# Kernel optimization log

Hardware: AMD Instinct MI355X
Metric: run time of the kernel (lower is better)

The kernel has to match this reference:

```python
import jax, jax.numpy as jnp
import numpy as np

N = 100000   # nodes
E = 1600000  # edges
D = 128      # feature dim (all layer_sizes equal)


def setup_inputs() -> dict:
    key = jax.random.key(0)
    ks = jax.random.split(key, 8)
    s = 1.0 / np.sqrt(D)
    return {
        "x": jax.random.normal(ks[0], (N, D), jnp.float32),
        "edge_index": jax.random.randint(ks[1], (2, E), 0, N, dtype=jnp.int32),
        "W1": jax.random.normal(ks[2], (D, D), jnp.float32) * s,  # GCNConv.lin weight [out,in]
        "b1": jnp.zeros((D,), jnp.float32),
        "a1": jnp.full((1,), 0.25, jnp.float32),  # PReLU slope (torch default)
        "W2": jax.random.normal(ks[3], (D, D), jnp.float32) * s,
        "b2": jnp.zeros((D,), jnp.float32),
        "a2": jnp.full((1,), 0.25, jnp.float32),
    }


def _gcn_conv(x, W, b, row, col, norm):
    # linear transform then normalized scatter-add aggregation
    h = x @ W.T + b                      # [N, D]
    msg = h[row] * norm[:, None]         # [E+N, D] gather + scale
    return jax.ops.segment_sum(msg, col, num_segments=N) # [N, D]


def _prelu(y, a):
    return jnp.where(y > 0, y, a * y)


def reference(x, edge_index, W1, b1, a1, W2, b2, a2):
    src, dst = edge_index[0], edge_index[1]
    loop = jnp.arange(N, dtype=src.dtype)
    # add self loops (GCNConv default add_self_loops=True)
    row = jnp.concatenate([src, loop])
    col = jnp.concatenate([dst, loop])
    # symmetric normalization: deg^{-1/2}[row] * deg^{-1/2}[col]
    deg = jax.ops.segment_sum(jnp.ones_like(col, dtype=x.dtype), col, num_segments=N)
    dis = jnp.where(deg > 0, jax.lax.rsqrt(deg), 0.0)
    norm = dis[row] * dis[col]
    # layer 1: GCNConv -> Identity (batchnorm=False) -> PReLU
    h = _prelu(_gcn_conv(x, W1, b1, row, col, norm), a1)
    # layer 2
    h = _prelu(_gcn_conv(h, W2, b2, row, col, norm), a2)
    return h
```

## Files before the change

### kernel.cpp

```cpp
#include <hip/hip_runtime.h>
#include <hip/hip_fp16.h>

#define D 128
#define PCH 4096

typedef _Float16 half_t;
typedef _Float16 f16x8 __attribute__((ext_vector_type(8)));
typedef _Float16 f16x4 __attribute__((ext_vector_type(4)));
typedef float    f32x4 __attribute__((ext_vector_type(4)));

__global__ __launch_bounds__(256) void k_histw(const int* __restrict__ dstv, int* bcnt,
                                               int e, int nb,
                                               const float* __restrict__ W1,
                                               const float* __restrict__ W2,
                                               half_t* __restrict__ Wh) {
    if (blockIdx.x >= 512) {
        int q = (blockIdx.x - 512) * 256 + threadIdx.x;
        if (q < 8192) {
            const float4* src = (q < 4096) ? (const float4*)W1 : (const float4*)W2;
            float4 v = src[q & 4095];
            f16x4 h;
            h[0] = (_Float16)v.x; h[1] = (_Float16)v.y;
            h[2] = (_Float16)v.z; h[3] = (_Float16)v.w;
            ((f16x4*)Wh)[q] = h;
        }
        return;
    }
    __shared__ int h[512];
    for (int i = threadIdx.x; i < nb; i += 256) h[i] = 0;
    __syncthreads();
    const int stride = 512 * 256;
    for (int i = blockIdx.x * 256 + threadIdx.x; i < e; i += stride)
        atomicAdd(&h[dstv[i] >> 8], 1);
    __syncthreads();
    for (int i = threadIdx.x; i < nb; i += 256)
        if (h[i]) atomicAdd(&bcnt[i], h[i]);
}

__global__ __launch_bounds__(512) void k_bscan(const int* __restrict__ bcnt, int* bbase,
                                               int* bcur, int nb, int e) {
    __shared__ int sd[512];
    int t = threadIdx.x;
    int v = (t < nb) ? bcnt[t] : 0;
    sd[t] = v;
    __syncthreads();
    for (int off = 1; off < 512; off <<= 1) {
        int x = (t >= off) ? sd[t - off] : 0;
        __syncthreads();
        sd[t] += x;
        __syncthreads();
    }
    int excl = sd[t] - v;
    if (t < nb) { bbase[t] = excl; bcur[t] = excl; }
    if (t == nb - 1) bbase[nb] = e;
}

__global__ __launch_bounds__(512) void k_part(const int* __restrict__ srcv,
                                              const int* __restrict__ dstv,
                                              int* bcur, unsigned int* __restrict__ ebuf,
                                              int e, int nb) {
    __shared__ int h[512];
    __shared__ int base[512];
    int c0 = blockIdx.x * PCH;
    int c1 = min(c0 + PCH, e);
    for (int i = threadIdx.x; i < nb; i += 512) h[i] = 0;
    __syncthreads();
    for (int i = c0 + threadIdx.x; i < c1; i += 512)
        atomicAdd(&h[dstv[i] >> 8], 1);
    __syncthreads();
    for (int i = threadIdx.x; i < nb; i += 512) {
        int c = h[i];
        base[i] = c ? atomicAdd(&bcur[i], c) : 0;
    }
    __syncthreads();
    for (int i = threadIdx.x; i < nb; i += 512) h[i] = 0;
    __syncthreads();
    for (int i = c0 + threadIdx.x; i < c1; i += 512) {
        int d = dstv[i];
        int b = d >> 8;
        int pos = atomicAdd(&h[b], 1);
        ebuf[base[b] + pos] = ((unsigned int)srcv[i] << 8) | (unsigned int)(d & 255);
    }
}

__global__ __launch_bounds__(512) void k_bucket(const unsigned int* __restrict__ ebuf,
                                                const int* __restrict__ bbase,
                                                int* __restrict__ rowptr,
                                                int* __restrict__ csr_src,
                                                float* __restrict__ dis, int n, int e) {
    __shared__ int cnt[256];
    __shared__ int off[256];
    int b = blockIdx.x;
    int t = threadIdx.x;
    int s0 = bbase[b], s1 = bbase[b + 1];
    if (t < 256) cnt[t] = 0;
    __syncthreads();
    for (int i = s0 + t; i < s1; i += 512)
        atomicAdd(&cnt[ebuf[i] & 255], 1);
    __syncthreads();
    int v = (t < 256) ? cnt[t] : 0;
    if (t < 256) off[t] = v;
    __syncthreads();
    for (int o = 1; o < 256; o <<= 1) {
        int x = (t >= o && t < 256) ? off[t - o] : 0;
        __syncthreads();
        if (t < 256) off[t] += x;
        __syncthreads();
    }
    if (t < 256) {
        int excl = off[t] - v;
        int node = b * 256 + t;
        if (node < n) {
            rowptr[node] = s0 + excl;
            dis[node] = rsqrtf((float)(v + 1));
        }
        if (b == 0 && t == 0) rowptr[n] = e;
        cnt[t] = excl;
    }
    __syncthreads();
    for (int i = s0 + t; i < s1; i += 512) {
        unsigned int u = ebuf[i];
        int pos = atomicAdd(&cnt[u & 255], 1);
        csr_src[s0 + pos] = (int)(u >> 8);
    }
}

template<bool FP16IN>
__global__ __launch_bounds__(512) void k_gemm(const void* __restrict__ Xv,
                                              const half_t* __restrict__ Wh,
                                              const float* __restrict__ B,
                                              const float* __restrict__ dis,
                                              half_t* __restrict__ Gh, int n) {
    __shared__ _Float16 lds[128 * 136];
    const int t = threadIdx.x;
    const int row0 = blockIdx.x * 128;

    #pragma unroll
    for (int i = 0; i < 4; ++i) {
        int gid = i * 512 + t;
        int row = gid >> 4, g = gid & 15;
        int grow = row0 + row;
        int so = ((g ^ (row & 7)) * 8);
        f16x8 hv;
        if constexpr (FP16IN) {
            uint4 u = make_uint4(0, 0, 0, 0);
            if (grow < n) u = ((const uint4*)Xv)[(size_t)grow * 16 + g];
            hv = *(f16x8*)&u;
        } else {
            float4 a = make_float4(0.f, 0.f, 0.f, 0.f);
            float4 b = make_float4(0.f, 0.f, 0.f, 0.f);
            if (grow < n) {
                a = ((const float4*)Xv)[(size_t)grow * 32 + g * 2];
                b = ((const float4*)Xv)[(size_t)grow * 32 + g * 2 + 1];
            }
            hv[0] = (_Float16)a.x; hv[1] = (_Float16)a.y;
            hv[2] = (_Float16)a.z; hv[3] = (_Float16)a.w;
            hv[4] = (_Float16)b.x; hv[5] = (_Float16)b.y;
            hv[6] = (_Float16)b.z; hv[7] = (_Float16)b.w;
        }
        *(f16x8*)&lds[row * 128 + so] = hv;
    }
    __syncthreads();

    const int w = t >> 6, l = t & 63;
    const int rbase = (w >> 1) * 32;
    const int cbase = (w & 1) * 64;
    const int lr = l & 15, lk = l >> 4;

    f32x4 acc[2][4] = {};

    #pragma unroll
    for (int kb = 0; kb < 4; ++kb) {
        f16x8 bf[4], af[2];
        #pragma unroll
        for (int ct = 0; ct < 4; ++ct) {
            int j = cbase + ct * 16 + lr;
            bf[ct] = *(const f16x8*)(Wh + j * 128 + kb * 32 + lk * 8);
        }
        #pragma unroll
        for (int rt = 0; rt < 2; ++rt) {
            int row = rbase + rt * 16 + lr;
            int G = kb * 4 + lk;
            af[rt] = *(const f16x8*)&lds[row * 128 + ((G ^ (row & 7)) * 8)];
        }
        #pragma unroll
        for (int rt = 0; rt < 2; ++rt)
            #pragma unroll
            for (int ct = 0; ct < 4; ++ct)
                acc[rt][ct] = __builtin_amdgcn_mfma_f32_16x16x32_f16(af[rt], bf[ct],
                                                                    acc[rt][ct], 0, 0, 0);
    }

    float bc[4];
    #pragma unroll
    for (int ct = 0; ct < 4; ++ct) bc[ct] = B[cbase + ct * 16 + lr];

    __syncthreads();
    #pragma unroll
    for (int rt = 0; rt < 2; ++rt)
        #pragma unroll
        for (int q = 0; q < 4; ++q) {
            int rl = rbase + rt * 16 + lk * 4 + q;
            int grow = row0 + rl;
            float ds = (grow < n) ? dis[grow] : 0.f;
            #pragma unroll
            for (int ct = 0; ct < 4; ++ct) {
                float v = (acc[rt][ct][q] + bc[ct]) * ds;
                lds[rl * 136 + cbase + ct * 16 + lr] = (_Float16)v;
            }
        }
    __syncthreads();
    #pragma unroll
    for (int i = 0; i < 4; ++i) {
        int gid = i * 512 + t;
        int row = gid >> 4, g = gid & 15;
        int grow = row0 + row;
        if (grow < n)
            *(f16x8*)&Gh[(size_t)grow * 128 + g * 8] = *(f16x8*)&lds[row * 136 + g * 8];
    }
}

template<bool FP16OUT>
__global__ __launch_bounds__(256) void k_gather(const half_t* __restrict__ G,
                                                const float* __restrict__ dis,
                                                const int* __restrict__ rowptr,
                                                const int* __restrict__ csr_src,
                                                const float* __restrict__ a,
                                                void* __restrict__ O, int n, int nquad) {
    int wq = (blockIdx.x * 256 + threadIdx.x) >> 6;
    if (wq >= nquad) return;
    int lane = threadIdx.x & 63;
    int node = wq * 4 + (lane >> 4);
    if (node >= n) node = n - 1;
    int sl = lane & 15;

    const uint4* Gv = (const uint4*)G;
    float ac[8];
    {
        uint4 su = Gv[(size_t)node * 16 + sl];
        f16x8 h = *(f16x8*)&su;
        #pragma unroll
        for (int j = 0; j < 8; ++j) ac[j] = (float)h[j];
    }

    int e = rowptr[node], e1 = rowptr[node + 1];
    for (; e + 4 <= e1; e += 4) {
        int s0 = csr_src[e + 0];
        int s1 = csr_src[e + 1];
        int s2 = csr_src[e + 2];
        int s3 = csr_src[e + 3];
        uint4 u0 = Gv[(size_t)s0 * 16 + sl];
        uint4 u1 = Gv[(size_t)s1 * 16 + sl];
        uint4 u2 = Gv[(size_t)s2 * 16 + sl];
        uint4 u3 = Gv[(size_t)s3 * 16 + sl];
        f16x8 h0 = *(f16x8*)&u0;
        f16x8 h1 = *(f16x8*)&u1;
        f16x8 h2 = *(f16x8*)&u2;
        f16x8 h3 = *(f16x8*)&u3;
        #pragma unroll
        for (int j = 0; j < 8; ++j)
            ac[j] += (float)h0[j] + (float)h1[j] + (float)h2[j] + (float)h3[j];
    }
    for (; e < e1; ++e) {
        int s = csr_src[e];
        uint4 u = Gv[(size_t)s * 16 + sl];
        f16x8 h = *(f16x8*)&u;
        #pragma unroll
        for (int j = 0; j < 8; ++j) ac[j] += (float)h[j];
    }

    float dsc = dis[node];
    float al = a[0];
    #pragma unroll
    for (int j = 0; j < 8; ++j) {
        float v = ac[j] * dsc;
        ac[j] = v > 0.f ? v : al * v;
    }
    if constexpr (FP16OUT) {
        f16x8 h;
        #pragma unroll
        for (int j = 0; j < 8; ++j) h[j] = (_Float16)ac[j];
        ((f16x8*)O)[(size_t)node * 16 + sl] = h;
    } else {
        float4 o0 = make_float4(ac[0], ac[1], ac[2], ac[3]);
        float4 o1 = make_float4(ac[4], ac[5], ac[6], ac[7]);
        ((float4*)O)[(size_t)node * 32 + sl * 2]     = o0;
        ((float4*)O)[(size_t)node * 32 + sl * 2 + 1] = o1;
    }
}

extern "C" void kernel_launch(void* const* d_in, const int* in_sizes, int n_in,
                              void* d_out, int out_size, void* d_ws, size_t ws_size,
                              hipStream_t stream) {
    const float* x  = (const float*)d_in[0];
    const int*   ei = (const int*)d_in[1];
    const float* W1 = (const float*)d_in[2];
    const float* b1 = (const float*)d_in[3];
    const float* a1 = (const float*)d_in[4];
    const float* W2 = (const float*)d_in[5];
    const float* b2 = (const float*)d_in[6];
    const float* a2 = (const float*)d_in[7];

    const int n = in_sizes[0] / D;
    const int e = in_sizes[1] / 2;
    const int* srcv = ei;
    const int* dstv = ei + e;
    const int nb = (n + 255) >> 8;

    char* ws = (char*)d_ws;
    size_t off = 0;
    auto alloc = [&](size_t bytes) {
        void* p = ws + off;
        off = (off + bytes + 255) & ~(size_t)255;
        return p;
    };
    float*        dis     = (float*)       alloc((size_t)n * 4);
    int*          rowptr  = (int*)         alloc((size_t)(n + 1) * 4);
    int*          csr_src = (int*)         alloc((size_t)e * 4);
    int*          bcnt    = (int*)         alloc(512 * 4);
    int*          bbase   = (int*)         alloc(513 * 4);
    int*          bcur    = (int*)         alloc(512 * 4);
    unsigned int* ebuf    = (unsigned int*)alloc((size_t)e * 4);
    half_t*       bufH    = (half_t*)      alloc((size_t)n * D * 2);
    half_t*       h1h     = (half_t*)      alloc((size_t)n * D * 2);
    half_t*       Wh      = (half_t*)      alloc(2 * 16384 * 2);

    dim3 blk(256);
    const int npart = (e + PCH - 1) / PCH;

    hipMemsetAsync(bcnt, 0, 512 * 4, stream);
    k_histw <<<544, blk, 0, stream>>>(dstv, bcnt, e, nb, W1, W2, Wh);
    k_bscan <<<1, 512, 0, stream>>>(bcnt, bbase, bcur, nb, e);
    k_part  <<<npart, 512, 0, stream>>>(srcv, dstv, bcur, ebuf, e, nb);
    k_bucket<<<nb, 512, 0, stream>>>(ebuf, bbase, rowptr, csr_src, dis, n, e);

    const int nquad = (n + 3) / 4;
    const int gat_grid = (nquad * 64 + 255) / 256;
    const int gemm_grid = (n + 127) / 128;

    k_gemm<false><<<gemm_grid, 512, 0, stream>>>(x, Wh, b1, dis, bufH, n);
    k_gather<true><<<gat_grid, blk, 0, stream>>>(bufH, dis, rowptr, csr_src, a1, h1h, n, nquad);
    k_gemm<true><<<gemm_grid, 512, 0, stream>>>(h1h, Wh + 16384, b2, dis, bufH, n);
    k_gather<false><<<gat_grid, blk, 0, stream>>>(bufH, dis, rowptr, csr_src, a2, d_out, n, nquad);
}
```

Baseline: 237.7 us.

## Fuse layer-1 gather with layer-2 GEMM and fold bucket scan into consumers

Folds the single-block bucket scan into k_part and k_bucket, which now each recompute the prefix sum of bucket counts redundantly. This removes one launch and the bbase buffer. It also fuses the layer-1 aggregation and PReLU with the layer-2 GEMM, so the aggregated features stay in LDS and are never written to and re-read from global memory. The cost is that the gather now runs at 128 rows per 512-thread block with a 16-lane-per-node layout, which may reduce the latency hiding available to the irregular gather loads.

Measured after the change: 245.6 us. 3.4% more time.

```diff
diff --git a/kernel.cpp b/kernel.cpp
--- a/kernel.cpp
+++ b/kernel.cpp
@@ -37,45 +37,42 @@
         if (h[i]) atomicAdd(&bcnt[i], h[i]);
 }
 
-__global__ __launch_bounds__(512) void k_bscan(const int* __restrict__ bcnt, int* bbase,
-                                               int* bcur, int nb, int e) {
+__global__ __launch_bounds__(512) void k_part(const int* __restrict__ srcv,
+                                              const int* __restrict__ dstv,
+                                              const int* __restrict__ bcnt,
+                                              int* bcur, unsigned int* __restrict__ ebuf,
+                                              int e, int nb) {
     __shared__ int sd[512];
+    __shared__ int bexcl[512];
+    __shared__ int h[512];
+    __shared__ int base[512];
     int t = threadIdx.x;
     int v = (t < nb) ? bcnt[t] : 0;
     sd[t] = v;
     __syncthreads();
-    for (int off = 1; off < 512; off <<= 1) {
-        int x = (t >= off) ? sd[t - off] : 0;
+    for (int o = 1; o < 512; o <<= 1) {
+        int x = (t >= o) ? sd[t - o] : 0;
         __syncthreads();
         sd[t] += x;
         __syncthreads();
     }
-    int excl = sd[t] - v;
-    if (t < nb) { bbase[t] = excl; bcur[t] = excl; }
-    if (t == nb - 1) bbase[nb] = e;
-}
-
-__global__ __launch_bounds__(512) void k_part(const int* __restrict__ srcv,
-                                              const int* __restrict__ dstv,
-                                              int* bcur, unsigned int* __restrict__ ebuf,
-                                              int e, int nb) {
-    __shared__ int h[512];
-    __shared__ int base[512];
+    bexcl[t] = sd[t] - v;
+    for (int i = t; i < nb; i += 512) h[i] = 0;
+    __syncthreads();
+
     int c0 = blockIdx.x * PCH;
     int c1 = min(c0 + PCH, e);
-    for (int i = threadIdx.x; i < nb; i += 512) h[i] = 0;
-    __syncthreads();
-    for (int i = c0 + threadIdx.x; i < c1; i += 512)
+    for (int i = c0 + t; i < c1; i += 512)
         atomicAdd(&h[dstv[i] >> 8], 1);
     __syncthreads();
-    for (int i = threadIdx.x; i < nb; i += 512) {
+    for (int i = t; i < nb; i += 512) {
         int c = h[i];
-        base[i] = c ? atomicAdd(&bcur[i], c) : 0;
-    }
-    __syncthreads();
-    for (int i = threadIdx.x; i < nb; i += 512) h[i] = 0;
-    __syncthreads();
-    for (int i = c0 + threadIdx.x; i < c1; i += 512) {
+        base[i] = c ? (bexcl[i] + atomicAdd(&bcur[i], c)) : 0;
+    }
+    __syncthreads();
+    for (int i = t; i < nb; i += 512) h[i] = 0;
+    __syncthreads();
+    for (int i = c0 + t; i < c1; i += 512) {
         int d = dstv[i];
         int b = d >> 8;
         int pos = atomicAdd(&h[b], 1);
@@ -84,15 +81,29 @@
 }
 
 __global__ __launch_bounds__(512) void k_bucket(const unsigned int* __restrict__ ebuf,
-                                                const int* __restrict__ bbase,
+                                                const int* __restrict__ bcnt,
                                                 int* __restrict__ rowptr,
                                                 int* __restrict__ csr_src,
-                                                float* __restrict__ dis, int n, int e) {
+                                                float* __restrict__ dis, int n, int e,
+                                                int nb) {
+    __shared__ int sd[512];
     __shared__ int cnt[256];
     __shared__ int off[256];
     int b = blockIdx.x;
     int t = threadIdx.x;
-    int s0 = bbase[b], s1 = bbase[b + 1];
+    int v0 = (t < nb) ? bcnt[t] : 0;
+    sd[t] = v0;
+    __syncthreads();
+    for (int o = 1; o < 512; o <<= 1) {
+        int x = (t >= o) ? sd[t - o] : 0;
+        __syncthreads();
+        sd[t] += x;
+        __syncthreads();
+    }
+    int s1 = sd[b];
+    int s0 = s1 - ((b < nb) ? bcnt[b] : 0);
+    __syncthreads();
+
     if (t < 256) cnt[t] = 0;
     __syncthreads();
     for (int i = s0 + t; i < s1; i += 512)
@@ -125,8 +136,7 @@
     }
 }
 
-template<bool FP16IN>
-__global__ __launch_bounds__(512) void k_gemm(const void* __restrict__ Xv,
+__global__ __launch_bounds__(512) void k_gemm(const float* __restrict__ Xv,
                                               const half_t* __restrict__ Wh,
                                               const float* __restrict__ B,
                                               const float* __restrict__ dis,
@@ -141,23 +151,17 @@
         int row = gid >> 4, g = gid & 15;
         int grow = row0 + row;
         int so = ((g ^ (row & 7)) * 8);
+        float4 a = make_float4(0.f, 0.f, 0.f, 0.f);
+        float4 b = make_float4(0.f, 0.f, 0.f, 0.f);
+        if (grow < n) {
+            a = ((const float4*)Xv)[(size_t)grow * 32 + g * 2];
+            b = ((const float4*)Xv)[(size_t)grow * 32 + g * 2 + 1];
+        }
         f16x8 hv;
-        if constexpr (FP16IN) {
-            uint4 u = make_uint4(0, 0, 0, 0);
-            if (grow < n) u = ((const uint4*)Xv)[(size_t)grow * 16 + g];
-            hv = *(f16x8*)&u;
-        } else {
-            float4 a = make_float4(0.f, 0.f, 0.f, 0.f);
-            float4 b = make_float4(0.f, 0.f, 0.f, 0.f);
-            if (grow < n) {
-                a = ((const float4*)Xv)[(size_t)grow * 32 + g * 2];
-                b = ((const float4*)Xv)[(size_t)grow * 32 + g * 2 + 1];
-            }
-            hv[0] = (_Float16)a.x; hv[1] = (_Float16)a.y;
-            hv[2] = (_Float16)a.z; hv[3] = (_Float16)a.w;
-            hv[4] = (_Float16)b.x; hv[5] = (_Float16)b.y;
-            hv[6] = (_Float16)b.z; hv[7] = (_Float16)b.w;
-        }
+        hv[0] = (_Float16)a.x; hv[1] = (_Float16)a.y;
+        hv[2] = (_Float16)a.z; hv[3] = (_Float16)a.w;
+        hv[4] = (_Float16)b.x; hv[5] = (_Float16)b.y;
+        hv[6] = (_Float16)b.z; hv[7] = (_Float16)b.w;
         *(f16x8*)&lds[row * 128 + so] = hv;
     }
     __syncthreads();
@@ -220,13 +224,137 @@
     }
 }
 
-template<bool FP16OUT>
+__global__ __launch_bounds__(512) void k_fusedg(const half_t* __restrict__ G1,
+                                                const float* __restrict__ dis,
+                                                const int* __restrict__ rowptr,
+                                                const int* __restrict__ csr_src,
+                                                const float* __restrict__ a,
+                                                const half_t* __restrict__ Wh,
+                                                const float* __restrict__ B,
+                                                half_t* __restrict__ G2, int n) {
+    __shared__ _Float16 lds[128 * 136];
+    const int t = threadIdx.x;
+    const int row0 = blockIdx.x * 128;
+    const int grp = t >> 4;
+    const int sl  = t & 15;
+    const float al = a[0];
+    const uint4* Gv = (const uint4*)G1;
+
+    #pragma unroll 1
+    for (int it = 0; it < 4; ++it) {
+        int rl = it * 32 + grp;
+        int node = row0 + rl;
+        float ac[8];
+        #pragma unroll
+        for (int j = 0; j < 8; ++j) ac[j] = 0.f;
+        if (node < n) {
+            uint4 su = Gv[(size_t)node * 16 + sl];
+            f16x8 h = *(f16x8*)&su;
+            #pragma unroll
+            for (int j = 0; j < 8; ++j) ac[j] = (float)h[j];
+            int e = rowptr[node], e1 = rowptr[node + 1];
+            for (; e + 4 <= e1; e += 4) {
+                int s0 = csr_src[e + 0];
+                int s1 = csr_src[e + 1];
+                int s2 = csr_src[e + 2];
+                int s3 = csr_src[e + 3];
+                uint4 u0 = Gv[(size_t)s0 * 16 + sl];
+                uint4 u1 = Gv[(size_t)s1 * 16 + sl];
+                uint4 u2 = Gv[(size_t)s2 * 16 + sl];
+                uint4 u3 = Gv[(size_t)s3 * 16 + sl];
+                f16x8 h0 = *(f16x8*)&u0;
+                f16x8 h1 = *(f16x8*)&u1;
+                f16x8 h2 = *(f16x8*)&u2;
+                f16x8 h3 = *(f16x8*)&u3;
+                #pragma unroll
+                for (int j = 0; j < 8; ++j)
+                    ac[j] += (float)h0[j] + (float)h1[j] + (float)h2[j] + (float)h3[j];
+            }
+            for (; e < e1; ++e) {
+                int s = csr_src[e];
+                uint4 u = Gv[(size_t)s * 16 + sl];
+                f16x8 h = *(f16x8*)&u;
+                #pragma unroll
+                for (int j = 0; j < 8; ++j) ac[j] += (float)h[j];
+            }
+            float dsc = dis[node];
+            #pragma unroll
+            for (int j = 0; j < 8; ++j) {
+                float v = ac[j] * dsc;
+                ac[j] = v > 0.f ? v : al * v;
+            }
+        }
+        f16x8 hv;
+        #pragma unroll
+        for (int j = 0; j < 8; ++j) hv[j] = (_Float16)ac[j];
+        *(f16x8*)&lds[rl * 128 + ((sl ^ (rl & 7)) * 8)] = hv;
+    }
+    __syncthreads();
+
+    const int w = t >> 6, l = t & 63;
+    const int rbase = (w >> 1) * 32;
+    const int cbase = (w & 1) * 64;
+    const int lr = l & 15, lk = l >> 4;
+
+    f32x4 acc[2][4] = {};
+
+    #pragma unroll
+    for (int kb = 0; kb < 4; ++kb) {
+        f16x8 bf[4], af[2];
+        #pragma unroll
+        for (int ct = 0; ct < 4; ++ct) {
+            int j = cbase + ct * 16 + lr;
+            bf[ct] = *(const f16x8*)(Wh + j * 128 + kb * 32 + lk * 8);
+        }
+        #pragma unroll
+        for (int rt = 0; rt < 2; ++rt) {
+            int row = rbase + rt * 16 + lr;
+            int G = kb * 4 + lk;
+            af[rt] = *(const f16x8*)&lds[row * 128 + ((G ^ (row & 7)) * 8)];
+        }
+        #pragma unroll
+        for (int rt = 0; rt < 2; ++rt)
+            #pragma unroll
+            for (int ct = 0; ct < 4; ++ct)
+                acc[rt][ct] = __builtin_amdgcn_mfma_f32_16x16x32_f16(af[rt], bf[ct],
+                                                                    acc[rt][ct], 0, 0, 0);
+    }
+
+    float bc[4];
+    #pragma unroll
+    for (int ct = 0; ct < 4; ++ct) bc[ct] = B[cbase + ct * 16 + lr];
+
+    __syncthreads();
+    #pragma unroll
+    for (int rt = 0; rt < 2; ++rt)
+        #pragma unroll
+        for (int q = 0; q < 4; ++q) {
+            int rl = rbase + rt * 16 + lk * 4 + q;
+            int grow = row0 + rl;
+            float ds = (grow < n) ? dis[grow] : 0.f;
+            #pragma unroll
+            for (int ct = 0; ct < 4; ++ct) {
+                float v = (acc[rt][ct][q] + bc[ct]) * ds;
+                lds[rl * 136 + cbase + ct * 16 + lr] = (_Float16)v;
+            }
+        }
+    __syncthreads();
+    #pragma unroll
+    for (int i = 0; i < 4; ++i) {
+        int gid = i * 512 + t;
+        int row = gid >> 4, g = gid & 15;
+        int grow = row0 + row;
+        if (grow < n)
+            *(f16x8*)&G2[(size_t)grow * 128 + g * 8] = *(f16x8*)&lds[row * 136 + g * 8];
+    }
+}
+
 __global__ __launch_bounds__(256) void k_gather(const half_t* __restrict__ G,
                                                 const float* __restrict__ dis,
                                                 const int* __restrict__ rowptr,
                                                 const int* __restrict__ csr_src,
                                                 const float* __restrict__ a,
-                                                void* __restrict__ O, int n, int nquad) {
+                                                float* __restrict__ O, int n, int nquad) {
     int wq = (blockIdx.x * 256 + threadIdx.x) >> 6;
     if (wq >= nquad) return;
     int lane = threadIdx.x & 63;
@@ -276,17 +404,10 @@
         float v = ac[j] * dsc;
         ac[j] = v > 0.f ? v : al * v;
     }
-    if constexpr (FP16OUT) {
-        f16x8 h;
-        #pragma unroll
-        for (int j = 0; j < 8; ++j) h[j] = (_Float16)ac[j];
-        ((f16x8*)O)[(size_t)node * 16 + sl] = h;
-    } else {
-        float4 o0 = make_float4(ac[0], ac[1], ac[2], ac[3]);
-        float4 o1 = make_float4(ac[4], ac[5], ac[6], ac[7]);
-        ((float4*)O)[(size_t)node * 32 + sl * 2]     = o0;
-        ((float4*)O)[(size_t)node * 32 + sl * 2 + 1] = o1;
-    }
+    float4 o0 = make_float4(ac[0], ac[1], ac[2], ac[3]);
+    float4 o1 = make_float4(ac[4], ac[5], ac[6], ac[7]);
+    ((float4*)O)[(size_t)node * 32 + sl * 2]     = o0;
+    ((float4*)O)[(size_t)node * 32 + sl * 2 + 1] = o1;
 }
 
 extern "C" void kernel_launch(void* const* d_in, const int* in_sizes, int n_in,
@@ -317,29 +438,28 @@
     float*        dis     = (float*)       alloc((size_t)n * 4);
     int*          rowptr  = (int*)         alloc((size_t)(n + 1) * 4);
     int*          csr_src = (int*)         alloc((size_t)e * 4);
-    int*          bcnt    = (int*)         alloc(512 * 4);
-    int*          bbase   = (int*)         alloc(513 * 4);
-    int*          bcur    = (int*)         alloc(512 * 4);
+    int*          bcnt    = (int*)         alloc(1024 * 4);
     unsigned int* ebuf    = (unsigned int*)alloc((size_t)e * 4);
-    half_t*       bufH    = (half_t*)      alloc((size_t)n * D * 2);
-    half_t*       h1h     = (half_t*)      alloc((size_t)n * D * 2);
+    half_t*       bufA    = (half_t*)      alloc((size_t)n * D * 2);
+    half_t*       bufB    = (half_t*)      alloc((size_t)n * D * 2);
     half_t*       Wh      = (half_t*)      alloc(2 * 16384 * 2);
+    int*          bcur    = bcnt + 512;
 
     dim3 blk(256);
     const int npart = (e + PCH - 1) / PCH;
 
-    hipMemsetAsync(bcnt, 0, 512 * 4, stream);
+    hipMemsetAsync(bcnt, 0, 1024 * 4, stream);
     k_histw <<<544, blk, 0, stream>>>(dstv, bcnt, e, nb, W1, W2, Wh);
-    k_bscan <<<1, 512, 0, stream>>>(bcnt, bbase, bcur, nb, e);
-    k_part  <<<npart, 512, 0, stream>>>(srcv, dstv, bcur, ebuf, e, nb);
-    k_bucket<<<nb, 512, 0, stream>>>(ebuf, bbase, rowptr, csr_src, dis, n, e);
+    k_part  <<<npart, 512, 0, stream>>>(srcv, dstv, bcnt, bcur, ebuf, e, nb);
+    k_bucket<<<nb, 512, 0, stream>>>(ebuf, bcnt, rowptr, csr_src, dis, n, e, nb);
 
     const int nquad = (n + 3) / 4;
     const int gat_grid = (nquad * 64 + 255) / 256;
     const int gemm_grid = (n + 127) / 128;
 
-    k_gemm<false><<<gemm_grid, 512, 0, stream>>>(x, Wh, b1, dis, bufH, n);
-    k_gather<true><<<gat_grid, blk, 0, stream>>>(bufH, dis, rowptr, csr_src, a1, h1h, n, nquad);
-    k_gemm<true><<<gemm_grid, 512, 0, stream>>>(h1h, Wh + 16384, b2, dis, bufH, n);
-    k_gather<false><<<gat_grid, blk, 0, stream>>>(bufH, dis, rowptr, csr_src, a2, d_out, n, nquad);
-}
+    k_gemm  <<<gemm_grid, 512, 0, stream>>>(x, Wh, b1, dis, bufA, n);
+    k_fusedg<<<gemm_grid, 512, 0, stream>>>(bufA, dis, rowptr, csr_src, a1,
+                                            Wh + 16384, b2, bufB, n);
+    k_gather<<<gat_grid, blk, 0, stream>>>(bufB, dis, rowptr, csr_src, a2,
+                                           (float*)d_out, n, nquad);
+}
```
